# Optimization experiments

Hardware: AMD Instinct MI355X
Metric: run time of the kernel (lower is better)

Reference implementation:

```python
import jax, jax.numpy as jnp
import numpy as np

N_SUBJECTS = 16
N_LABELS = 8
DENS_TEMP = 0.1  # args.ProtoSim_dens_temp


def setup_inputs() -> dict:
    key = jax.random.key(0)
    k1, k2, k3 = jax.random.split(key, 3)
    B, V, D = 131072, 2, 128
    X_data = jax.random.normal(k1, (B, V, D), dtype=jnp.float32)
    subject = jax.random.randint(k2, (B,), 0, N_SUBJECTS, dtype=jnp.int64) if jax.config.read('jax_enable_x64') else jax.random.randint(k2, (B,), 0, N_SUBJECTS)
    labels = jax.random.randint(k3, (B,), 0, N_LABELS)
    return {"X_data": X_data, "subject": subject, "labels": labels}


def reference(X_data, subject, labels):
    B, V, D = X_data.shape
    G = N_SUBJECTS * N_LABELS
    # torch.cat(torch.unbind(X_data, dim=1), dim=0): view-major ordering -> [V*B, D]
    cf = jnp.transpose(X_data, (1, 0, 2)).reshape(V * B, D)
    # subject/labels duplicated once (module assumes 2 views)
    seg = jnp.tile(subject * N_LABELS + labels, V)  # group id per row, [V*B]
    counts = jax.ops.segment_sum(jnp.ones((V * B,), jnp.float32), seg, num_segments=G)
    centroid = jax.ops.segment_sum(cf, seg, num_segments=G) / counts[:, None]  # [G, D]
    # per-point euclidean distance to own group centroid (torch.cdist to 1-row centroid)
    dist = jnp.linalg.norm(cf - centroid[seg], axis=1)  # [V*B]
    # density: mean(sqrt(dist)) / log(n + 10) for groups with n > 1, else 0 then dmax
    dens = (jax.ops.segment_sum(jnp.sqrt(dist), seg, num_segments=G) / counts) / jnp.log(counts + 10.0)
    dens = jnp.where(counts > 1, dens, 0.0)
    dens = jnp.where(counts > 1, dens, dens.max())
    lo = jnp.percentile(dens, 10.0)
    hi = jnp.percentile(dens, 90.0)
    dens = jnp.clip(dens, lo, hi)
    dens = DENS_TEMP * dens / dens.mean()
    cen_of_cen = centroid.mean(axis=0)  # [D]
    sim = jnp.exp((centroid @ cen_of_cen) / dens)  # [G]
    sim = sim - sim.max()
    return -sim.mean()
```

## Files before the change

kernel.cpp:

```cpp
#include <hip/hip_runtime.h>
#include <cstdint>
#include <cstddef>

#define BPTS  131072
#define D_DIM 128
#define G_GR  128
#define NL    8
#define NSLC  16
#define PERMBUF 256
#define NBLK_S  64
#define PTS_PER (BPTS / NBLK_S)

__global__ __launch_bounds__(256) void k_hist_blk(const int* __restrict__ sub,
                                                  const int* __restrict__ lab,
                                                  int* __restrict__ hblk) {
    __shared__ int h[G_GR];
    int t = threadIdx.x, blk = blockIdx.x;
    if (t < G_GR) h[t] = 0;
    __syncthreads();
    int base = blk * PTS_PER;
    for (int i = t; i < PTS_PER; i += 256)
        atomicAdd(&h[sub[base + i] * NL + lab[base + i]], 1);
    __syncthreads();
    if (t < G_GR) hblk[blk * G_GR + t] = h[t];
}

__global__ __launch_bounds__(128) void k_prefix(const int* __restrict__ hblk,
                                                int* __restrict__ counts,
                                                int* __restrict__ offsets,
                                                int* __restrict__ base,
                                                float* __restrict__ countsf) {
    __shared__ int tot[G_GR];
    int t = threadIdx.x;
    int s = 0;
    for (int b = 0; b < NBLK_S; ++b) s += hblk[b * G_GR + t];
    tot[t] = s;
    counts[t] = s;
    countsf[t] = 2.0f * (float)s;
    __syncthreads();
    int o = 0;
    for (int j = 0; j < t; ++j) o += tot[j];
    offsets[t] = o;
    int run = o;
    for (int b = 0; b < NBLK_S; ++b) {
        base[b * G_GR + t] = run;
        run += hblk[b * G_GR + t];
    }
}

__global__ __launch_bounds__(256) void k_scatter(const int* __restrict__ sub,
                                                 const int* __restrict__ lab,
                                                 const int* __restrict__ base,
                                                 int* __restrict__ perm) {
    __shared__ int cur[G_GR];
    int t = threadIdx.x, blk = blockIdx.x;
    if (t < G_GR) cur[t] = base[blk * G_GR + t];
    __syncthreads();
    int b0 = blk * PTS_PER;
    for (int i = t; i < PTS_PER; i += 256) {
        int p = b0 + i;
        int g = sub[p] * NL + lab[p];
        int s = atomicAdd(&cur[g], 1);
        perm[s] = p;
    }
}

__global__ __launch_bounds__(256) void k_psum(const float4* __restrict__ X4,
                                              const int* __restrict__ perm,
                                              const int* __restrict__ offsets,
                                              const int* __restrict__ counts,
                                              float* __restrict__ part) {
    __shared__ int   pbuf[PERMBUF];
    __shared__ float red[4 * 256];
    int g = blockIdx.x / NSLC, s = blockIdx.x % NSLC;
    int off = offsets[g], len = counts[g];
    int lo = off + (int)(((long)len * s) / NSLC);
    int hi = off + (int)(((long)len * (s + 1)) / NSLC);
    int slen = hi - lo;
    int t = threadIdx.x, lane = t & 63, w = t >> 6;

    for (int j = t; j < slen; j += 256) pbuf[j] = perm[lo + j];
    __syncthreads();

    float4 acc = make_float4(0.f, 0.f, 0.f, 0.f);
    for (int i = w * 8; i < slen; i += 32) {
#pragma unroll
        for (int u = 0; u < 8; ++u) {
            int j  = i + u;
            int jj = (j < slen) ? j : (slen - 1);
            int b  = pbuf[jj];
            float4 x = X4[(size_t)b * 64 + lane];
            if (j < slen) { acc.x += x.x; acc.y += x.y; acc.z += x.z; acc.w += x.w; }
        }
    }
    red[w * 256 + lane * 4 + 0] = acc.x;
    red[w * 256 + lane * 4 + 1] = acc.y;
    red[w * 256 + lane * 4 + 2] = acc.z;
    red[w * 256 + lane * 4 + 3] = acc.w;
    __syncthreads();
    if (t < 128) {
        float v = 0.f;
        for (int r = 0; r < 4; ++r) v += red[r * 256 + t] + red[r * 256 + t + 128];
        part[(size_t)(g * NSLC + s) * 128 + t] = v;
    }
}

__global__ __launch_bounds__(256) void k_reduce(const float* __restrict__ part,
                                                const int* __restrict__ counts,
                                                float* __restrict__ centroid) {
    int t = blockIdx.x * 256 + threadIdx.x;
    if (t >= G_GR * D_DIM) return;
    int g = t >> 7, d = t & 127;
    float v = 0.f;
    for (int s = 0; s < NSLC; ++s) v += part[(size_t)(g * NSLC + s) * 128 + d];
    int n = counts[g];
    centroid[t] = (n > 0) ? v / (2.0f * (float)n) : 0.f;
}

__global__ __launch_bounds__(256) void k_dist(const float4* __restrict__ X4,
                                              const int* __restrict__ perm,
                                              const int* __restrict__ offsets,
                                              const int* __restrict__ counts,
                                              const float* __restrict__ centroid,
                                              float* __restrict__ dpart) {
    __shared__ int   pbuf[PERMBUF];
    __shared__ float cen[D_DIM];
    __shared__ float wsum[4];
    int g = blockIdx.x / NSLC, s = blockIdx.x % NSLC;
    int off = offsets[g], len = counts[g];
    int lo = off + (int)(((long)len * s) / NSLC);
    int hi = off + (int)(((long)len * (s + 1)) / NSLC);
    int slen = hi - lo;
    int t = threadIdx.x, lane = t & 63, w = t >> 6;

    for (int j = t; j < slen; j += 256) pbuf[j] = perm[lo + j];
    if (t < D_DIM) cen[t] = centroid[g * D_DIM + t];
    __syncthreads();

    int cd = (lane * 4) & 127;
    float4 c = make_float4(cen[cd], cen[cd + 1], cen[cd + 2], cen[cd + 3]);

    float sacc = 0.f;
    for (int i = w * 8; i < slen; i += 32) {
#pragma unroll
        for (int u = 0; u < 8; ++u) {
            int j  = i + u;
            int jj = (j < slen) ? j : (slen - 1);
            int b  = pbuf[jj];
            float4 x = X4[(size_t)b * 64 + lane];
            float dx = x.x - c.x, dy = x.y - c.y, dz = x.z - c.z, dw = x.w - c.w;
            float d = dx * dx + dy * dy + dz * dz + dw * dw;
#pragma unroll
            for (int m = 1; m <= 16; m <<= 1) d += __shfl_xor(d, m);
            if (j < slen) sacc += sqrtf(sqrtf(d));
        }
    }
    float tot = sacc + __shfl_xor(sacc, 32);
    if (lane == 0) wsum[w] = tot;
    __syncthreads();
    if (t == 0) {
        float v = 0.f;
        for (int r = 0; r < 4; ++r) v += wsum[r];
        dpart[g * NSLC + s] = v;
    }
}

__global__ __launch_bounds__(128) void k_final(const float* __restrict__ dpart,
                                               const float* __restrict__ countsf,
                                               const float* __restrict__ centroid,
                                               float* __restrict__ out) {
    __shared__ float srt[G_GR];
    __shared__ float red[G_GR];
    __shared__ float coc[D_DIM];
    int t = threadIdx.x;

    float ds = 0.f;
    for (int s = 0; s < NSLC; ++s) ds += dpart[t * NSLC + s];
    float cnt  = countsf[t];
    float dens = (cnt > 1.f) ? (ds / cnt) / logf(cnt + 10.f) : 0.f;

    red[t] = dens;
    __syncthreads();
    for (int s = 64; s > 0; s >>= 1) {
        if (t < s) red[t] = fmaxf(red[t], red[t + s]);
        __syncthreads();
    }
    float dmax = red[0];
    __syncthreads();
    if (!(cnt > 1.f)) dens = dmax;

    srt[t] = dens;
    __syncthreads();
    for (int k = 2; k <= G_GR; k <<= 1) {
        for (int j = k >> 1; j > 0; j >>= 1) {
            int ixj = t ^ j;
            if (ixj > t) {
                float a = srt[t], b = srt[ixj];
                bool up = ((t & k) == 0);
                if ((a > b) == up) { srt[t] = b; srt[ixj] = a; }
            }
            __syncthreads();
        }
    }
    double p10 = 0.10 * 127.0, p90 = 0.90 * 127.0;
    int   i10 = (int)p10,           i90 = (int)p90;
    float f10 = (float)(p10 - i10), f90 = (float)(p90 - i90);
    float lo = srt[i10] + f10 * (srt[i10 + 1] - srt[i10]);
    float hi = srt[i90] + f90 * (srt[i90 + 1] - srt[i90]);
    dens = fminf(fmaxf(dens, lo), hi);

    red[t] = dens;
    __syncthreads();
    for (int s = 64; s > 0; s >>= 1) {
        if (t < s) red[t] += red[t + s];
        __syncthreads();
    }
    float dmean = red[0] / 128.f;
    __syncthreads();
    dens = 0.1f * dens / dmean;

    float cs = 0.f;
    for (int g = 0; g < G_GR; ++g) cs += centroid[g * D_DIM + t];
    coc[t] = cs / 128.f;
    __syncthreads();

    float dot = 0.f;
    for (int d = 0; d < D_DIM; ++d) dot += centroid[t * D_DIM + d] * coc[d];
    float sim = expf(dot / dens);

    red[t] = sim;
    __syncthreads();
    for (int s = 64; s > 0; s >>= 1) {
        if (t < s) red[t] = fmaxf(red[t], red[t + s]);
        __syncthreads();
    }
    float smax = red[0];
    __syncthreads();
    red[t] = sim - smax;
    __syncthreads();
    for (int s = 64; s > 0; s >>= 1) {
        if (t < s) red[t] += red[t + s];
        __syncthreads();
    }
    if (t == 0) out[0] = -(red[0] / 128.f);
}

extern "C" void kernel_launch(void* const* d_in, const int* in_sizes, int n_in,
                              void* d_out, int out_size, void* d_ws, size_t ws_size,
                              hipStream_t stream) {
    const float* X       = (const float*)d_in[0];
    const int*   subject = (const int*)d_in[1];
    const int*   labels  = (const int*)d_in[2];
    float*       out     = (float*)d_out;
    char*        ws      = (char*)d_ws;

    size_t o = 0;
    int*   counts   = (int*)(ws + o);   o += 512;
    int*   offsets  = (int*)(ws + o);   o += 512;
    float* countsf  = (float*)(ws + o); o += 512;
    int*   hblk     = (int*)(ws + o);   o += (size_t)NBLK_S * G_GR * 4;
    int*   base     = (int*)(ws + o);   o += (size_t)NBLK_S * G_GR * 4;
    int*   perm     = (int*)(ws + o);   o += (size_t)BPTS * 4;
    float* part     = (float*)(ws + o); o += (size_t)G_GR * NSLC * 128 * 4;
    float* centroid = (float*)(ws + o); o += (size_t)G_GR * D_DIM * 4;
    float* dpart    = (float*)(ws + o); o += (size_t)G_GR * NSLC * 4;

    k_hist_blk<<<NBLK_S, 256, 0, stream>>>(subject, labels, hblk);
    k_prefix  <<<1, 128, 0, stream>>>(hblk, counts, offsets, base, countsf);
    k_scatter <<<NBLK_S, 256, 0, stream>>>(subject, labels, base, perm);
    k_psum    <<<G_GR * NSLC, 256, 0, stream>>>((const float4*)X, perm, offsets, counts, part);
    k_reduce  <<<(G_GR * D_DIM + 255) / 256, 256, 0, stream>>>(part, counts, centroid);
    k_dist    <<<G_GR * NSLC, 256, 0, stream>>>((const float4*)X, perm, offsets, counts, centroid, dpart);
    k_final   <<<1, 128, 0, stream>>>(dpart, countsf, centroid, out);
}
```

Measured before the change: 244.6 us.

## Fuse prefix into scatter and reduce into dist; batch gather loads

The single-block prefix kernel is folded into the scatter kernel: each block recomputes the group totals and its own per-block base offsets from the histogram. The partial-sum reduction that builds the centroids is folded into the start of the distance kernel, so two launches and their round-trips through global memory go away. The psum and dist inner loops now issue all eight gathered float4 loads before consuming any of them, which puts more memory requests in flight. In exchange there is redundant work: every scatter block re-reads the full histogram, and all sixteen slice blocks of a group recompute the same centroid. PERMBUF is cut to 128, which still covers the expected slice length of about 64.

```diff
diff --git a/kernel.cpp b/kernel.cpp
--- a/kernel.cpp
+++ b/kernel.cpp
@@ -2,62 +2,63 @@
 #include <cstdint>
 #include <cstddef>
 
-#define BPTS  131072
-#define D_DIM 128
-#define G_GR  128
-#define NL    8
-#define NSLC  16
-#define PERMBUF 256
+#define BPTS    131072
+#define D_DIM   128
+#define G_GR    128
+#define NL      8
+#define NSLC    16
+#define PERMBUF 128
 #define NBLK_S  64
-#define PTS_PER (BPTS / NBLK_S)
-
-__global__ __launch_bounds__(256) void k_hist_blk(const int* __restrict__ sub,
-                                                  const int* __restrict__ lab,
-                                                  int* __restrict__ hblk) {
+#define PPB     (BPTS / NBLK_S)
+
+__global__ __launch_bounds__(256) void k_hist(const int* __restrict__ sub,
+                                              const int* __restrict__ lab,
+                                              int* __restrict__ hblk) {
     __shared__ int h[G_GR];
     int t = threadIdx.x, blk = blockIdx.x;
     if (t < G_GR) h[t] = 0;
     __syncthreads();
-    int base = blk * PTS_PER;
-    for (int i = t; i < PTS_PER; i += 256)
-        atomicAdd(&h[sub[base + i] * NL + lab[base + i]], 1);
+    int b0 = blk * PPB;
+    for (int i = t; i < PPB; i += 256)
+        atomicAdd(&h[sub[b0 + i] * NL + lab[b0 + i]], 1);
     __syncthreads();
     if (t < G_GR) hblk[blk * G_GR + t] = h[t];
-}
-
-__global__ __launch_bounds__(128) void k_prefix(const int* __restrict__ hblk,
-                                                int* __restrict__ counts,
-                                                int* __restrict__ offsets,
-                                                int* __restrict__ base,
-                                                float* __restrict__ countsf) {
-    __shared__ int tot[G_GR];
-    int t = threadIdx.x;
-    int s = 0;
-    for (int b = 0; b < NBLK_S; ++b) s += hblk[b * G_GR + t];
-    tot[t] = s;
-    counts[t] = s;
-    countsf[t] = 2.0f * (float)s;
-    __syncthreads();
-    int o = 0;
-    for (int j = 0; j < t; ++j) o += tot[j];
-    offsets[t] = o;
-    int run = o;
-    for (int b = 0; b < NBLK_S; ++b) {
-        base[b * G_GR + t] = run;
-        run += hblk[b * G_GR + t];
-    }
 }
 
 __global__ __launch_bounds__(256) void k_scatter(const int* __restrict__ sub,
                                                  const int* __restrict__ lab,
-                                                 const int* __restrict__ base,
+                                                 const int* __restrict__ hblk,
+                                                 int* __restrict__ counts,
+                                                 int* __restrict__ offsets,
+                                                 float* __restrict__ countsf,
                                                  int* __restrict__ perm) {
+    __shared__ int tot[G_GR];
     __shared__ int cur[G_GR];
     int t = threadIdx.x, blk = blockIdx.x;
-    if (t < G_GR) cur[t] = base[blk * G_GR + t];
-    __syncthreads();
-    int b0 = blk * PTS_PER;
-    for (int i = t; i < PTS_PER; i += 256) {
+    if (t < G_GR) {
+        int tt = 0, mine = 0;
+        for (int b = 0; b < NBLK_S; ++b) {
+            int v = hblk[b * G_GR + t];
+            tt += v;
+            if (b < blk) mine += v;
+        }
+        tot[t] = tt;
+        cur[t] = mine;
+    }
+    __syncthreads();
+    if (t < G_GR) {
+        int off = 0;
+        for (int j = 0; j < t; ++j) off += tot[j];
+        cur[t] += off;
+        if (blk == 0) {
+            counts[t]  = tot[t];
+            offsets[t] = off;
+            countsf[t] = 2.0f * (float)tot[t];
+        }
+    }
+    __syncthreads();
+    int b0 = blk * PPB;
+    for (int i = t; i < PPB; i += 256) {
         int p = b0 + i;
         int g = sub[p] * NL + lab[p];
         int s = atomicAdd(&cur[g], 1);
@@ -72,10 +73,10 @@
                                               float* __restrict__ part) {
     __shared__ int   pbuf[PERMBUF];
     __shared__ float red[4 * 256];
-    int g = blockIdx.x / NSLC, s = blockIdx.x % NSLC;
+    int g = blockIdx.x >> 4, s = blockIdx.x & 15;
     int off = offsets[g], len = counts[g];
-    int lo = off + (int)(((long)len * s) / NSLC);
-    int hi = off + (int)(((long)len * (s + 1)) / NSLC);
+    int lo = off + (len * s) / NSLC;
+    int hi = off + (len * (s + 1)) / NSLC;
     int slen = hi - lo;
     int t = threadIdx.x, lane = t & 63, w = t >> 6;
 
@@ -84,13 +85,21 @@
 
     float4 acc = make_float4(0.f, 0.f, 0.f, 0.f);
     for (int i = w * 8; i < slen; i += 32) {
-#pragma unroll
-        for (int u = 0; u < 8; ++u) {
-            int j  = i + u;
-            int jj = (j < slen) ? j : (slen - 1);
-            int b  = pbuf[jj];
-            float4 x = X4[(size_t)b * 64 + lane];
-            if (j < slen) { acc.x += x.x; acc.y += x.y; acc.z += x.z; acc.w += x.w; }
+        int idx[8];
+#pragma unroll
+        for (int u = 0; u < 8; ++u) {
+            int j = i + u;
+            idx[u] = pbuf[(j < slen) ? j : (slen - 1)];
+        }
+        float4 x[8];
+#pragma unroll
+        for (int u = 0; u < 8; ++u) x[u] = X4[(size_t)idx[u] * 64 + lane];
+#pragma unroll
+        for (int u = 0; u < 8; ++u) {
+            if (i + u < slen) {
+                acc.x += x[u].x; acc.y += x[u].y;
+                acc.z += x[u].z; acc.w += x[u].w;
+            }
         }
     }
     red[w * 256 + lane * 4 + 0] = acc.x;
@@ -100,69 +109,68 @@
     __syncthreads();
     if (t < 128) {
         float v = 0.f;
-        for (int r = 0; r < 4; ++r) v += red[r * 256 + t] + red[r * 256 + t + 128];
-        part[(size_t)(g * NSLC + s) * 128 + t] = v;
-    }
-}
-
-__global__ __launch_bounds__(256) void k_reduce(const float* __restrict__ part,
-                                                const int* __restrict__ counts,
-                                                float* __restrict__ centroid) {
-    int t = blockIdx.x * 256 + threadIdx.x;
-    if (t >= G_GR * D_DIM) return;
-    int g = t >> 7, d = t & 127;
-    float v = 0.f;
-    for (int s = 0; s < NSLC; ++s) v += part[(size_t)(g * NSLC + s) * 128 + d];
-    int n = counts[g];
-    centroid[t] = (n > 0) ? v / (2.0f * (float)n) : 0.f;
+        for (int r = 0; r < 4; ++r)
+            v += red[r * 256 + t] + red[r * 256 + t + 128];
+        part[(size_t)blockIdx.x * 128 + t] = v;
+    }
 }
 
 __global__ __launch_bounds__(256) void k_dist(const float4* __restrict__ X4,
                                               const int* __restrict__ perm,
                                               const int* __restrict__ offsets,
                                               const int* __restrict__ counts,
-                                              const float* __restrict__ centroid,
+                                              const float* __restrict__ part,
+                                              float* __restrict__ centroid,
                                               float* __restrict__ dpart) {
     __shared__ int   pbuf[PERMBUF];
     __shared__ float cen[D_DIM];
     __shared__ float wsum[4];
-    int g = blockIdx.x / NSLC, s = blockIdx.x % NSLC;
+    int g = blockIdx.x >> 4, s = blockIdx.x & 15;
     int off = offsets[g], len = counts[g];
-    int lo = off + (int)(((long)len * s) / NSLC);
-    int hi = off + (int)(((long)len * (s + 1)) / NSLC);
+    int lo = off + (len * s) / NSLC;
+    int hi = off + (len * (s + 1)) / NSLC;
     int slen = hi - lo;
     int t = threadIdx.x, lane = t & 63, w = t >> 6;
 
+    if (t < D_DIM) {
+        float v = 0.f;
+        for (int s2 = 0; s2 < NSLC; ++s2)
+            v += part[(size_t)(g * NSLC + s2) * 128 + t];
+        float c = (len > 0) ? v / (2.0f * (float)len) : 0.f;
+        cen[t] = c;
+        if (s == 0) centroid[g * D_DIM + t] = c;
+    }
     for (int j = t; j < slen; j += 256) pbuf[j] = perm[lo + j];
-    if (t < D_DIM) cen[t] = centroid[g * D_DIM + t];
-    __syncthreads();
-
-    int cd = (lane * 4) & 127;
+    __syncthreads();
+
+    int cd = (lane & 31) * 4;
     float4 c = make_float4(cen[cd], cen[cd + 1], cen[cd + 2], cen[cd + 3]);
 
     float sacc = 0.f;
     for (int i = w * 8; i < slen; i += 32) {
-#pragma unroll
-        for (int u = 0; u < 8; ++u) {
-            int j  = i + u;
-            int jj = (j < slen) ? j : (slen - 1);
-            int b  = pbuf[jj];
-            float4 x = X4[(size_t)b * 64 + lane];
-            float dx = x.x - c.x, dy = x.y - c.y, dz = x.z - c.z, dw = x.w - c.w;
+        int idx[8];
+#pragma unroll
+        for (int u = 0; u < 8; ++u) {
+            int j = i + u;
+            idx[u] = pbuf[(j < slen) ? j : (slen - 1)];
+        }
+        float4 x[8];
+#pragma unroll
+        for (int u = 0; u < 8; ++u) x[u] = X4[(size_t)idx[u] * 64 + lane];
+#pragma unroll
+        for (int u = 0; u < 8; ++u) {
+            float dx = x[u].x - c.x, dy = x[u].y - c.y;
+            float dz = x[u].z - c.z, dw = x[u].w - c.w;
             float d = dx * dx + dy * dy + dz * dz + dw * dw;
 #pragma unroll
             for (int m = 1; m <= 16; m <<= 1) d += __shfl_xor(d, m);
-            if (j < slen) sacc += sqrtf(sqrtf(d));
-        }
-    }
-    float tot = sacc + __shfl_xor(sacc, 32);
-    if (lane == 0) wsum[w] = tot;
-    __syncthreads();
-    if (t == 0) {
-        float v = 0.f;
-        for (int r = 0; r < 4; ++r) v += wsum[r];
-        dpart[g * NSLC + s] = v;
-    }
+            if (i + u < slen) sacc += sqrtf(sqrtf(d));
+        }
+    }
+    float t2 = sacc + __shfl_xor(sacc, 32);
+    if (lane == 0) wsum[w] = t2;
+    __syncthreads();
+    if (t == 0) dpart[blockIdx.x] = wsum[0] + wsum[1] + wsum[2] + wsum[3];
 }
 
 __global__ __launch_bounds__(128) void k_final(const float* __restrict__ dpart,
@@ -248,28 +256,25 @@
 extern "C" void kernel_launch(void* const* d_in, const int* in_sizes, int n_in,
                               void* d_out, int out_size, void* d_ws, size_t ws_size,
                               hipStream_t stream) {
-    const float* X       = (const float*)d_in[0];
-    const int*   subject = (const int*)d_in[1];
-    const int*   labels  = (const int*)d_in[2];
-    float*       out     = (float*)d_out;
-    char*        ws      = (char*)d_ws;
+    const float4* X4      = (const float4*)d_in[0];
+    const int*    subject = (const int*)d_in[1];
+    const int*    labels  = (const int*)d_in[2];
+    float*        out     = (float*)d_out;
+    char*         ws      = (char*)d_ws;
 
     size_t o = 0;
+    int*   hblk     = (int*)(ws + o);   o += (size_t)NBLK_S * G_GR * 4;
     int*   counts   = (int*)(ws + o);   o += 512;
     int*   offsets  = (int*)(ws + o);   o += 512;
     float* countsf  = (float*)(ws + o); o += 512;
-    int*   hblk     = (int*)(ws + o);   o += (size_t)NBLK_S * G_GR * 4;
-    int*   base     = (int*)(ws + o);   o += (size_t)NBLK_S * G_GR * 4;
     int*   perm     = (int*)(ws + o);   o += (size_t)BPTS * 4;
     float* part     = (float*)(ws + o); o += (size_t)G_GR * NSLC * 128 * 4;
     float* centroid = (float*)(ws + o); o += (size_t)G_GR * D_DIM * 4;
     float* dpart    = (float*)(ws + o); o += (size_t)G_GR * NSLC * 4;
 
-    k_hist_blk<<<NBLK_S, 256, 0, stream>>>(subject, labels, hblk);
-    k_prefix  <<<1, 128, 0, stream>>>(hblk, counts, offsets, base, countsf);
-    k_scatter <<<NBLK_S, 256, 0, stream>>>(subject, labels, base, perm);
-    k_psum    <<<G_GR * NSLC, 256, 0, stream>>>((const float4*)X, perm, offsets, counts, part);
-    k_reduce  <<<(G_GR * D_DIM + 255) / 256, 256, 0, stream>>>(part, counts, centroid);
-    k_dist    <<<G_GR * NSLC, 256, 0, stream>>>((const float4*)X, perm, offsets, counts, centroid, dpart);
-    k_final   <<<1, 128, 0, stream>>>(dpart, countsf, centroid, out);
-}
+    k_hist   <<<NBLK_S, 256, 0, stream>>>(subject, labels, hblk);
+    k_scatter<<<NBLK_S, 256, 0, stream>>>(subject, labels, hblk, counts, offsets, countsf, perm);
+    k_psum   <<<G_GR * NSLC, 256, 0, stream>>>(X4, perm, offsets, counts, part);
+    k_dist   <<<G_GR * NSLC, 256, 0, stream>>>(X4, perm, offsets, counts, part, centroid, dpart);
+    k_final  <<<1, 128, 0, stream>>>(dpart, countsf, centroid, out);
+}
```

Result: no change. 242.8 us (-0.7%).
